# Kernel optimization log

Measured on AMD Instinct MI355X. Metric: run time of the kernel, lower is better.

The kernel has to match this reference:

```python
import jax, jax.numpy as jnp
import numpy as np

N = 100_000          # nodes
E = 1_600_000        # edges
NUM_LABELS = 1000
LBL_DIM = 64
BBOX_DIM = 64        # bbox MLP output dim
HID = 128            # gnn hidden = out channels; gnn in = LBL_DIM + BBOX_DIM = 128


def setup_inputs() -> dict:
    key = jax.random.key(0)
    ks = jax.random.split(key, 14)
    label = jax.random.randint(ks[0], (N,), 0, NUM_LABELS)
    bbox = jax.random.uniform(ks[1], (N, 4), dtype=jnp.float32)
    edge_index = jax.random.randint(ks[2], (2, E), 0, N)
    emb_table = jax.random.normal(ks[3], (NUM_LABELS, LBL_DIM), dtype=jnp.float32) * 0.02
    mlp_w1 = jax.random.normal(ks[4], (4, BBOX_DIM), dtype=jnp.float32) * 0.5
    mlp_b1 = jnp.zeros((BBOX_DIM,), jnp.float32)
    mlp_w2 = jax.random.normal(ks[5], (BBOX_DIM, BBOX_DIM), dtype=jnp.float32) * 0.125
    mlp_b2 = jnp.zeros((BBOX_DIM,), jnp.float32)
    w_g0 = jax.random.normal(ks[6], (HID, HID), dtype=jnp.float32) * 0.088
    b_g0 = jnp.zeros((HID,), jnp.float32)
    w_g1 = jax.random.normal(ks[7], (HID, HID), dtype=jnp.float32) * 0.088
    b_g1 = jnp.zeros((HID,), jnp.float32)
    w_g2 = jax.random.normal(ks[8], (HID, HID), dtype=jnp.float32) * 0.088
    b_g2 = jnp.zeros((HID,), jnp.float32)
    return dict(label=label, bbox=bbox, edge_index=edge_index, emb_table=emb_table,
                mlp_w1=mlp_w1, mlp_b1=mlp_b1, mlp_w2=mlp_w2, mlp_b2=mlp_b2,
                w_g0=w_g0, b_g0=b_g0, w_g1=w_g1, b_g1=b_g1, w_g2=w_g2, b_g2=b_g2)


def _gcn_norm(edge_index, n):
    # add self loops, compute symmetric normalization deg^-1/2 A_hat deg^-1/2
    loops = jnp.arange(n, dtype=edge_index.dtype)
    src = jnp.concatenate([edge_index[0], loops])
    dst = jnp.concatenate([edge_index[1], loops])
    deg = jax.ops.segment_sum(jnp.ones_like(dst, dtype=jnp.float32), dst, num_segments=n)
    dinv = jnp.where(deg > 0, jax.lax.rsqrt(deg), 0.0)
    norm = dinv[src] * dinv[dst]  # [E+N]
    return src, dst, norm


def _gcn_conv(x, src, dst, norm, w, b, n):
    h = x @ w                                   # [N, C]
    msg = h[src] * norm[:, None]                # gather + scale, [E+N, C]
    out = jax.ops.segment_sum(msg, dst, num_segments=n)  # scatter-add
    return out + b


def reference(label, bbox, edge_index, emb_table,
              mlp_w1, mlp_b1, mlp_w2, mlp_b2,
              w_g0, b_g0, w_g1, b_g1, w_g2, b_g2):
    n = bbox.shape[0]
    lbl = emb_table[label]                                  # [N, 64]
    h = jax.nn.relu(bbox @ mlp_w1 + mlp_b1) @ mlp_w2 + mlp_b2  # [N, 64]
    x = jnp.concatenate([lbl, h], axis=-1)                  # [N, 128]
    src, dst, norm = _gcn_norm(edge_index, n)
    x = jax.nn.relu(_gcn_conv(x, src, dst, norm, w_g0, b_g0, n))
    x = jax.nn.relu(_gcn_conv(x, src, dst, norm, w_g1, b_g1, n))
    x = _gcn_conv(x, src, dst, norm, w_g2, b_g2, n)
    return x
```

## Files before the change

### kernel.cpp

```cpp
#include <hip/hip_runtime.h>
#include <hip/hip_bf16.h>
#include <hip/hip_fp16.h>
#include <cstdint>
#include <cstddef>

typedef _Float16 h8 __attribute__((ext_vector_type(8)));
typedef float f4 __attribute__((ext_vector_type(4)));

#define CNT_PAD 16


__global__ __launch_bounds__(256) void k_count_rank(const int* __restrict__ dst, int* __restrict__ cnt_pad,
                                                    int* __restrict__ rank, int E) {
    int i = blockIdx.x * 256 + threadIdx.x;
    if (i < E) rank[i] = atomicAdd(&cnt_pad[(size_t)dst[i] * CNT_PAD], 1);
}

__global__ __launch_bounds__(256) void k_scan_a(const int* __restrict__ cnt_pad, int* __restrict__ offs,
                                                int* __restrict__ partials, float* __restrict__ dinv,
                                                int* __restrict__ blockHist, int N, int nb) {
    __shared__ int sh[256];
    __shared__ int lh[64];
    int t = threadIdx.x;
    if (t < 64) lh[t] = 0;
    int i = blockIdx.x * 256 + t;
    int v = (i < N) ? (cnt_pad[(size_t)i * CNT_PAD] + 1) : 0;
    sh[t] = v;
    __syncthreads();
    if (i < N) {
        int b = v < 64 ? v : 63;
        atomicAdd(&lh[b], 1);
    }
    for (int d = 1; d < 256; d <<= 1) {
        int add = (t >= d) ? sh[t - d] : 0;
        __syncthreads();
        sh[t] += add;
        __syncthreads();
    }
    if (i < N) {
        offs[i] = sh[t] - v;
        dinv[i] = rsqrtf((float)v);
    }
    if (t == 255) partials[blockIdx.x] = sh[255];
    __syncthreads();
    if (t < 64) blockHist[(size_t)t * nb + blockIdx.x] = lh[t];
}

__global__ __launch_bounds__(256) void k_scan_bins(int* __restrict__ blockHist, int* __restrict__ hist, int nb) {
    __shared__ int sh[256];
    int b = blockIdx.x;
    int* p = blockHist + (size_t)b * nb;
    int t = threadIdx.x;
    int carry = 0;
    for (int base = 0; base < nb; base += 256) {
        int idx = base + t;
        int v = idx < nb ? p[idx] : 0;
        sh[t] = v;
        __syncthreads();
        for (int d = 1; d < 256; d <<= 1) {
            int add = (t >= d) ? sh[t - d] : 0;
            __syncthreads();
            sh[t] += add;
            __syncthreads();
        }
        if (idx < nb) p[idx] = carry + sh[t] - v;
        carry += sh[255];
        __syncthreads();
    }
    if (t == 0) hist[b * CNT_PAD] = carry;
}

__global__ __launch_bounds__(512) void k_scan_b(int* __restrict__ partials, int* __restrict__ hist, int nb) {
    __shared__ int sh[512];
    __shared__ int hs[64];
    int t = threadIdx.x;
    int v = (t < nb) ? partials[t] : 0;
    sh[t] = v;
    if (t < 64) hs[t] = hist[t * CNT_PAD];
    __syncthreads();
    for (int d = 1; d < 512; d <<= 1) {
        int add = (t >= d) ? sh[t - d] : 0;
        __syncthreads();
        sh[t] += add;
        __syncthreads();
    }
    if (t < nb) partials[t] = sh[t];
    for (int d = 1; d < 64; d <<= 1) {
        int add = (t >= d && t < 64) ? hs[t - d] : 0;
        __syncthreads();
        if (t < 64) hs[t] += add;
        __syncthreads();
    }
    if (t < 64) hist[t * CNT_PAD] = t ? hs[t - 1] : 0;
}

__global__ __launch_bounds__(256) void k_scan_c(int* __restrict__ offs, const int* __restrict__ partials,
                                                const int* __restrict__ cnt_pad, const float* __restrict__ dinv,
                                                long long* __restrict__ cpack, int N, int nb) {
    int i = blockIdx.x * 256 + threadIdx.x;
    if (i < N) {
        int b = i >> 8;
        int o = offs[i] + (b > 0 ? partials[b - 1] : 0);
        offs[i] = o;
        int cnt = cnt_pad[(size_t)i * CNT_PAD];
        float di = dinv[i];
        unsigned int nrm = (unsigned int)__float_as_int(di * di);
        long long v = ((long long)nrm << 32) | (unsigned int)i;
        __builtin_nontemporal_store(v, &cpack[o + cnt]);
    } else if (i == N) {
        offs[N] = partials[nb - 1];
    }
}

__global__ __launch_bounds__(256) void k_fill2(const int* __restrict__ src, const int* __restrict__ dst,
                                               const int* __restrict__ rank, const int* __restrict__ offs,
                                               const float* __restrict__ dinv,
                                               long long* __restrict__ cpack, int E) {
    int i = blockIdx.x * 256 + threadIdx.x;
    if (i < E) {
        int s = src[i], d = dst[i];
        int pos = offs[d] + rank[i];
        unsigned int nrm = (unsigned int)__float_as_int(dinv[s] * dinv[d]);
        long long v = ((long long)nrm << 32) | (unsigned int)s;
        __builtin_nontemporal_store(v, &cpack[pos]);
    }
}

__global__ __launch_bounds__(256) void k_perm_scatter2(const int* __restrict__ cnt_pad,
                                                       const int* __restrict__ hist,
                                                       const int* __restrict__ blockBinOff,
                                                       int* __restrict__ perm, int N, int nb) {
    __shared__ int lh[64];
    int t = threadIdx.x;
    if (t < 64) lh[t] = 0;
    __syncthreads();
    int i = blockIdx.x * 256 + t;
    if (i < N) {
        int deg = cnt_pad[(size_t)i * CNT_PAD] + 1;
        int b = deg < 64 ? deg : 63;
        int lr = atomicAdd(&lh[b], 1);
        int pos = hist[b * CNT_PAD] + blockBinOff[(size_t)b * nb + blockIdx.x] + lr;
        perm[pos] = i;
    }
}


__global__ __launch_bounds__(256) void k_prep_w(const float* __restrict__ w0, const float* __restrict__ w1,
                                                const float* __restrict__ w2, _Float16* __restrict__ WT) {
    int idx = blockIdx.x * 256 + threadIdx.x;
    if (idx >= 3 * 16384) return;
    int l = idx >> 14, rem = idx & 16383, c = rem >> 7, k = rem & 127;
    const float* W = (l == 0) ? w0 : (l == 1) ? w1 : w2;
    WT[idx] = (_Float16)W[k * 128 + c];
}


__global__ __launch_bounds__(256) void k_feat_gemm(const int* __restrict__ label, const float* __restrict__ bbox,
                                                   const float* __restrict__ emb,
                                                   const float* __restrict__ w1, const float* __restrict__ b1,
                                                   const float* __restrict__ w2, const float* __restrict__ b2,
                                                   const _Float16* __restrict__ WT0,
                                                   _Float16* __restrict__ G0, int N) {
    __shared__ float w1s[256];
    __shared__ float b1s[64], b2s[64];
    __shared__ _Float16 w2t[64][72];
    __shared__ _Float16 h1s[32][72];
    __shared__ _Float16 Fl[32][136];

    int t = threadIdx.x;
    if (t < 256) w1s[t] = w1[t];
    if (t < 64) { b1s[t] = b1[t]; b2s[t] = b2[t]; }
    #pragma unroll
    for (int i = 0; i < 16; ++i) {
        int idx = t + i * 256;
        int k = idx >> 6, c = idx & 63;
        w2t[c][k] = (_Float16)w2[idx];
    }

    int wv = t >> 6, lane = t & 63;
    int r = lane & 15, q = lane >> 4;
    int blockBase = blockIdx.x * 32;
    int nb0 = blockBase + wv * 8;

    #pragma unroll
    for (int nn = 0; nn < 8; ++nn) {
        int node = nb0 + nn;
        float h1 = 0.f;
        _Float16 ev = (_Float16)0.f;
        if (node < N) {
            float bb0 = bbox[node * 4 + 0];
            float bb1 = bbox[node * 4 + 1];
            float bb2 = bbox[node * 4 + 2];
            float bb3 = bbox[node * 4 + 3];
            h1 = fmaxf(bb0 * w1s[lane] + bb1 * w1s[64 + lane]
                     + bb2 * w1s[128 + lane] + bb3 * w1s[192 + lane] + b1s[lane], 0.f);
            ev = (_Float16)emb[(size_t)label[node] * 64 + lane];
        }
        h1s[wv * 8 + nn][lane] = (_Float16)h1;
        Fl[wv * 8 + nn][lane] = ev;
    }
    __syncthreads();

    int rt = wv & 1, ch = wv >> 1;
    {
        h8 a0 = *(const h8*)&h1s[rt * 16 + r][q * 8];
        h8 a1 = *(const h8*)&h1s[rt * 16 + r][32 + q * 8];
        #pragma unroll
        for (int ct = 0; ct < 2; ++ct) {
            int col = ch * 32 + ct * 16 + r;
            h8 bv0 = *(const h8*)&w2t[col][q * 8];
            h8 bv1 = *(const h8*)&w2t[col][32 + q * 8];
            f4 acc = {0.f, 0.f, 0.f, 0.f};
            acc = __builtin_amdgcn_mfma_f32_16x16x32_f16(a0, bv0, acc, 0, 0, 0);
            acc = __builtin_amdgcn_mfma_f32_16x16x32_f16(a1, bv1, acc, 0, 0, 0);
            float bb = b2s[col];
            #pragma unroll
            for (int i = 0; i < 4; ++i)
                Fl[rt * 16 + q * 4 + i][64 + col] = (_Float16)(acc[i] + bb);
        }
    }
    __syncthreads();

    {
        h8 a[4];
        #pragma unroll
        for (int s = 0; s < 4; ++s) a[s] = *(const h8*)&Fl[rt * 16 + r][s * 32 + q * 8];
        #pragma unroll
        for (int ct = 0; ct < 4; ++ct) {
            int col = ch * 64 + ct * 16 + r;
            f4 acc = {0.f, 0.f, 0.f, 0.f};
            #pragma unroll
            for (int s = 0; s < 4; ++s) {
                h8 bv = *(const h8*)&WT0[(size_t)col * 128 + s * 32 + q * 8];
                acc = __builtin_amdgcn_mfma_f32_16x16x32_f16(a[s], bv, acc, 0, 0, 0);
            }
            #pragma unroll
            for (int i = 0; i < 4; ++i) {
                int node = blockBase + rt * 16 + q * 4 + i;
                if (node < N) G0[(size_t)node * 128 + col] = (_Float16)acc[i];
            }
        }
    }
}


__global__ __launch_bounds__(256) void k_gemm_mfma(const _Float16* __restrict__ X,
                                                   const _Float16* __restrict__ WT,
                                                   _Float16* __restrict__ H, int N) {
    int t = threadIdx.x;
    int wv = t >> 6, lane = t & 63;
    int r = lane & 15, q = lane >> 4;
    int n0 = blockIdx.x * 64 + wv * 16;

    int arow = n0 + r; if (arow > N - 1) arow = N - 1;
    h8 a[4];
    #pragma unroll
    for (int s = 0; s < 4; ++s)
        a[s] = *(const h8*)&X[(size_t)arow * 128 + s * 32 + q * 8];

    #pragma unroll
    for (int ct = 0; ct < 8; ++ct) {
        h8 b[4];
        #pragma unroll
        for (int s = 0; s < 4; ++s)
            b[s] = *(const h8*)&WT[(size_t)(ct * 16 + r) * 128 + s * 32 + q * 8];
        f4 acc = {0.f, 0.f, 0.f, 0.f};
        #pragma unroll
        for (int s = 0; s < 4; ++s)
            acc = __builtin_amdgcn_mfma_f32_16x16x32_f16(a[s], b[s], acc, 0, 0, 0);
        #pragma unroll
        for (int i = 0; i < 4; ++i) {
            int row = n0 + q * 4 + i;
            if (row < N) H[(size_t)row * 128 + ct * 16 + r] = (_Float16)acc[i];
        }
    }
}


#define FMA8(hv, wv_)                                                                        \
    {                                                                                        \
        float2 f;                                                                            \
        f = __half22float2(*(const __half2*)&(hv).x); acc[0] += f.x * (wv_); acc[1] += f.y * (wv_); \
        f = __half22float2(*(const __half2*)&(hv).y); acc[2] += f.x * (wv_); acc[3] += f.y * (wv_); \
        f = __half22float2(*(const __half2*)&(hv).z); acc[4] += f.x * (wv_); acc[5] += f.y * (wv_); \
        f = __half22float2(*(const __half2*)&(hv).w); acc[6] += f.x * (wv_); acc[7] += f.y * (wv_); \
    }

template <int OUT_HALF>
__global__ __launch_bounds__(256) void k_agg(const uint4* __restrict__ H4, const int* __restrict__ offs,
                                             const int2* __restrict__ cpack, const int* __restrict__ perm,
                                             const float* __restrict__ bias, void* __restrict__ Yv,
                                             int N, int do_relu) {
    int slot = blockIdx.x * 16 + (threadIdx.x >> 4);
    if (slot >= N) return;
    int node = perm[slot];
    int li = threadIdx.x & 15;
    int i0 = offs[node], i1 = offs[node + 1];

    float acc[8];
    #pragma unroll
    for (int k = 0; k < 8; ++k) acc[k] = 0.f;

    for (int base = i0; base < i1; base += 16) {
        int navail = i1 - base; if (navail > 16) navail = 16;
        int lidx = li < navail ? li : (navail - 1);
        int2 ep = cpack[base + lidx];

        float wA[4]; uint4 hA[4];
        #pragma unroll
        for (int j = 0; j < 4; ++j) {
            int cl = j < navail ? j : (navail - 1);
            int s = __shfl(ep.x, cl, 16);
            float wj = __int_as_float(__shfl(ep.y, cl, 16));
            wA[j] = j < navail ? wj : 0.f;
            hA[j] = H4[(size_t)s * 16 + li];
        }
        for (int e = 4; e < navail; e += 4) {
            float wB[4]; uint4 hB[4];
            #pragma unroll
            for (int j = 0; j < 4; ++j) {
                int idx = e + j;
                int cl = idx < navail ? idx : (navail - 1);
                int s = __shfl(ep.x, cl, 16);
                float wj = __int_as_float(__shfl(ep.y, cl, 16));
                wB[j] = idx < navail ? wj : 0.f;
                hB[j] = H4[(size_t)s * 16 + li];
            }
            #pragma unroll
            for (int j = 0; j < 4; ++j) FMA8(hA[j], wA[j]);
            #pragma unroll
            for (int j = 0; j < 4; ++j) { wA[j] = wB[j]; hA[j] = hB[j]; }
        }
        #pragma unroll
        for (int j = 0; j < 4; ++j) FMA8(hA[j], wA[j]);
    }

    float4 b0 = *(const float4*)&bias[li * 8];
    float4 b1 = *(const float4*)&bias[li * 8 + 4];
    acc[0] += b0.x; acc[1] += b0.y; acc[2] += b0.z; acc[3] += b0.w;
    acc[4] += b1.x; acc[5] += b1.y; acc[6] += b1.z; acc[7] += b1.w;
    if (do_relu) {
        #pragma unroll
        for (int k = 0; k < 8; ++k) acc[k] = fmaxf(acc[k], 0.f);
    }
    if (OUT_HALF) {
        __half2 p0 = __float22half2_rn(make_float2(acc[0], acc[1]));
        __half2 p1 = __float22half2_rn(make_float2(acc[2], acc[3]));
        __half2 p2 = __float22half2_rn(make_float2(acc[4], acc[5]));
        __half2 p3 = __float22half2_rn(make_float2(acc[6], acc[7]));
        uint4 pk;
        pk.x = *(unsigned int*)&p0; pk.y = *(unsigned int*)&p1;
        pk.z = *(unsigned int*)&p2; pk.w = *(unsigned int*)&p3;
        ((uint4*)Yv)[(size_t)node * 16 + li] = pk;
    } else {
        float* Yf = (float*)Yv;
        *(float4*)&Yf[(size_t)node * 128 + li * 8]     = make_float4(acc[0], acc[1], acc[2], acc[3]);
        *(float4*)&Yf[(size_t)node * 128 + li * 8 + 4] = make_float4(acc[4], acc[5], acc[6], acc[7]);
    }
}


extern "C" void kernel_launch(void* const* d_in, const int* in_sizes, int n_in,
                              void* d_out, int out_size, void* d_ws, size_t ws_size,
                              hipStream_t stream) {
    const int*   label = (const int*)d_in[0];
    const float* bbox  = (const float*)d_in[1];
    const int*   eidx  = (const int*)d_in[2];
    const float* emb   = (const float*)d_in[3];
    const float* w1    = (const float*)d_in[4];
    const float* b1    = (const float*)d_in[5];
    const float* w2    = (const float*)d_in[6];
    const float* b2    = (const float*)d_in[7];
    const float* wg0   = (const float*)d_in[8];
    const float* bg0   = (const float*)d_in[9];
    const float* wg1   = (const float*)d_in[10];
    const float* bg1   = (const float*)d_in[11];
    const float* wg2   = (const float*)d_in[12];
    const float* bg2   = (const float*)d_in[13];

    int N = in_sizes[0];
    int E = in_sizes[2] / 2;
    const int* esrc = eidx;
    const int* edst = eidx + E;

    char* ws = (char*)d_ws;
    int*       offs      = (int*)      (ws + 0x000000);
    float*     dinv      = (float*)    (ws + 0x070000);
    int*       perm      = (int*)      (ws + 0x0E0000);
    int*       partials  = (int*)      (ws + 0x150000);
    int*       hist      = (int*)      (ws + 0x158000);
    _Float16*  WT        = (_Float16*) (ws + 0x160000);
    int*       blockBinOff = (int*)    (ws + 0x180000);
    long long* cpack     = (long long*)(ws + 0x200000);
    __half*    B         = (__half*)   (ws + 0x1000000);
    int*       cnt_pad   = (int*)      (ws + 0x1000000);
    int*       rank      = (int*)      (ws + 0x1800000);
    __half*    A         = (__half*)   (ws + 0x2900000);
    float*     Of        = (float*)    d_out;

    int nb = (N + 255) / 256;
    int eb = (E + 255) / 256;

    hipMemsetAsync(cnt_pad, 0, (size_t)N * CNT_PAD * 4, stream);
    k_count_rank<<<eb, 256, 0, stream>>>(edst, cnt_pad, rank, E);
    k_scan_a<<<nb, 256, 0, stream>>>(cnt_pad, offs, partials, dinv, blockBinOff, N, nb);
    k_scan_bins<<<64, 256, 0, stream>>>(blockBinOff, hist, nb);
    k_scan_b<<<1, 512, 0, stream>>>(partials, hist, nb);
    k_scan_c<<<(N + 1 + 255) / 256, 256, 0, stream>>>(offs, partials, cnt_pad, dinv, cpack, N, nb);
    k_fill2<<<eb, 256, 0, stream>>>(esrc, edst, rank, offs, dinv, cpack, E);
    k_perm_scatter2<<<nb, 256, 0, stream>>>(cnt_pad, hist, blockBinOff, perm, N, nb);

    k_prep_w<<<192, 256, 0, stream>>>(wg0, wg1, wg2, WT);
    k_feat_gemm<<<(N + 31) / 32, 256, 0, stream>>>(label, bbox, emb, w1, b1, w2, b2,
                                                   WT + 0 * 16384, (_Float16*)A, N);

    int gemm_grid = (N + 63) / 64;
    int agg_grid  = (N + 15) / 16;

    k_agg<1><<<agg_grid, 256, 0, stream>>>((const uint4*)A, offs, (const int2*)cpack, perm, bg0, B, N, 1);
    k_gemm_mfma<<<gemm_grid, 256, 0, stream>>>((const _Float16*)B, WT + 1 * 16384, (_Float16*)A, N);
    k_agg<1><<<agg_grid, 256, 0, stream>>>((const uint4*)A, offs, (const int2*)cpack, perm, bg1, B, N, 1);
    k_gemm_mfma<<<gemm_grid, 256, 0, stream>>>((const _Float16*)B, WT + 2 * 16384, (_Float16*)A, N);
    k_agg<0><<<agg_grid, 256, 0, stream>>>((const uint4*)A, offs, (const int2*)cpack, perm, bg2, Of, N, 0);
}
```

Baseline: 441.8 us.

## Fuse GCN aggregation with next-layer MFMA GEMM and batch edge preprocessing

```diff
diff --git a/kernel.cpp b/kernel.cpp
--- a/kernel.cpp
+++ b/kernel.cpp
@@ -12,8 +12,22 @@
 
 __global__ __launch_bounds__(256) void k_count_rank(const int* __restrict__ dst, int* __restrict__ cnt_pad,
                                                     int* __restrict__ rank, int E) {
-    int i = blockIdx.x * 256 + threadIdx.x;
-    if (i < E) rank[i] = atomicAdd(&cnt_pad[(size_t)dst[i] * CNT_PAD], 1);
+    int G = gridDim.x * 256;
+    int g = blockIdx.x * 256 + threadIdx.x;
+    int idx[4], d[4]; bool v[4];
+    #pragma unroll
+    for (int k = 0; k < 4; ++k) {
+        idx[k] = g + k * G;
+        v[k] = idx[k] < E;
+        d[k] = v[k] ? dst[idx[k]] : 0;
+    }
+    int r[4];
+    #pragma unroll
+    for (int k = 0; k < 4; ++k)
+        if (v[k]) r[k] = atomicAdd(&cnt_pad[(size_t)d[k] * CNT_PAD], 1);
+    #pragma unroll
+    for (int k = 0; k < 4; ++k)
+        if (v[k]) rank[idx[k]] = r[k];
 }
 
 __global__ __launch_bounds__(256) void k_scan_a(const int* __restrict__ cnt_pad, int* __restrict__ offs,
@@ -116,13 +130,29 @@
                                                const int* __restrict__ rank, const int* __restrict__ offs,
                                                const float* __restrict__ dinv,
                                                long long* __restrict__ cpack, int E) {
-    int i = blockIdx.x * 256 + threadIdx.x;
-    if (i < E) {
-        int s = src[i], d = dst[i];
-        int pos = offs[d] + rank[i];
-        unsigned int nrm = (unsigned int)__float_as_int(dinv[s] * dinv[d]);
-        long long v = ((long long)nrm << 32) | (unsigned int)s;
-        __builtin_nontemporal_store(v, &cpack[pos]);
+    int G = gridDim.x * 256;
+    int g = blockIdx.x * 256 + threadIdx.x;
+    int idx[4], s[4], d[4], rk[4]; bool v[4];
+    #pragma unroll
+    for (int k = 0; k < 4; ++k) {
+        idx[k] = g + k * G;
+        v[k] = idx[k] < E;
+        int safe = v[k] ? idx[k] : 0;
+        s[k] = src[safe]; d[k] = dst[safe]; rk[k] = rank[safe];
+    }
+    int pos[4]; float ds[4], dd[4];
+    #pragma unroll
+    for (int k = 0; k < 4; ++k) {
+        pos[k] = offs[d[k]] + rk[k];
+        ds[k] = dinv[s[k]]; dd[k] = dinv[d[k]];
+    }
+    #pragma unroll
+    for (int k = 0; k < 4; ++k) {
+        if (v[k]) {
+            unsigned int nrm = (unsigned int)__float_as_int(ds[k] * dd[k]);
+            long long val = ((long long)nrm << 32) | (unsigned int)s[k];
+            __builtin_nontemporal_store(val, &cpack[pos[k]]);
+        }
     }
 }
 
@@ -244,39 +274,6 @@
 }
 
 
-__global__ __launch_bounds__(256) void k_gemm_mfma(const _Float16* __restrict__ X,
-                                                   const _Float16* __restrict__ WT,
-                                                   _Float16* __restrict__ H, int N) {
-    int t = threadIdx.x;
-    int wv = t >> 6, lane = t & 63;
-    int r = lane & 15, q = lane >> 4;
-    int n0 = blockIdx.x * 64 + wv * 16;
-
-    int arow = n0 + r; if (arow > N - 1) arow = N - 1;
-    h8 a[4];
-    #pragma unroll
-    for (int s = 0; s < 4; ++s)
-        a[s] = *(const h8*)&X[(size_t)arow * 128 + s * 32 + q * 8];
-
-    #pragma unroll
-    for (int ct = 0; ct < 8; ++ct) {
-        h8 b[4];
-        #pragma unroll
-        for (int s = 0; s < 4; ++s)
-            b[s] = *(const h8*)&WT[(size_t)(ct * 16 + r) * 128 + s * 32 + q * 8];
-        f4 acc = {0.f, 0.f, 0.f, 0.f};
-        #pragma unroll
-        for (int s = 0; s < 4; ++s)
-            acc = __builtin_amdgcn_mfma_f32_16x16x32_f16(a[s], b[s], acc, 0, 0, 0);
-        #pragma unroll
-        for (int i = 0; i < 4; ++i) {
-            int row = n0 + q * 4 + i;
-            if (row < N) H[(size_t)row * 128 + ct * 16 + r] = (_Float16)acc[i];
-        }
-    }
-}
-
-
 #define FMA8(hv, wv_)                                                                        \
     {                                                                                        \
         float2 f;                                                                            \
@@ -286,76 +283,109 @@
         f = __half22float2(*(const __half2*)&(hv).w); acc[6] += f.x * (wv_); acc[7] += f.y * (wv_); \
     }
 
-template <int OUT_HALF>
-__global__ __launch_bounds__(256) void k_agg(const uint4* __restrict__ H4, const int* __restrict__ offs,
-                                             const int2* __restrict__ cpack, const int* __restrict__ perm,
-                                             const float* __restrict__ bias, void* __restrict__ Yv,
-                                             int N, int do_relu) {
-    int slot = blockIdx.x * 16 + (threadIdx.x >> 4);
-    if (slot >= N) return;
-    int node = perm[slot];
-    int li = threadIdx.x & 15;
-    int i0 = offs[node], i1 = offs[node + 1];
+template <int MODE>
+__global__ __launch_bounds__(256) void k_agg_gemm(const uint4* __restrict__ H4, const int* __restrict__ offs,
+                                                  const int2* __restrict__ cpack,
+                                                  const int* __restrict__ perm,
+                                                  const float* __restrict__ bias,
+                                                  const _Float16* __restrict__ WTnext,
+                                                  void* __restrict__ Yv, int N) {
+    __shared__ _Float16 Zl[16][136];
+    __shared__ int nid[16];
+
+    int t = threadIdx.x;
+    int grp = t >> 4;
+    int li = t & 15;
+    int blockBase = blockIdx.x * 16;
+    int slot = blockBase + grp;
+    int node;
+    if (MODE == 1) node = slot < N ? perm[slot] : -1;
+    else           node = slot < N ? slot : -1;
+    if (MODE == 1 && li == 0) nid[grp] = node;
 
     float acc[8];
     #pragma unroll
     for (int k = 0; k < 8; ++k) acc[k] = 0.f;
 
-    for (int base = i0; base < i1; base += 16) {
-        int navail = i1 - base; if (navail > 16) navail = 16;
-        int lidx = li < navail ? li : (navail - 1);
-        int2 ep = cpack[base + lidx];
-
-        float wA[4]; uint4 hA[4];
-        #pragma unroll
-        for (int j = 0; j < 4; ++j) {
-            int cl = j < navail ? j : (navail - 1);
-            int s = __shfl(ep.x, cl, 16);
-            float wj = __int_as_float(__shfl(ep.y, cl, 16));
-            wA[j] = j < navail ? wj : 0.f;
-            hA[j] = H4[(size_t)s * 16 + li];
-        }
-        for (int e = 4; e < navail; e += 4) {
-            float wB[4]; uint4 hB[4];
+    if (node >= 0) {
+        int i0 = offs[node], i1 = offs[node + 1];
+        for (int base = i0; base < i1; base += 16) {
+            int navail = i1 - base; if (navail > 16) navail = 16;
+            int lidx = li < navail ? li : (navail - 1);
+            int2 ep = cpack[base + lidx];
+
+            float wA[4]; uint4 hA[4];
             #pragma unroll
             for (int j = 0; j < 4; ++j) {
-                int idx = e + j;
-                int cl = idx < navail ? idx : (navail - 1);
+                int cl = j < navail ? j : (navail - 1);
                 int s = __shfl(ep.x, cl, 16);
                 float wj = __int_as_float(__shfl(ep.y, cl, 16));
-                wB[j] = idx < navail ? wj : 0.f;
-                hB[j] = H4[(size_t)s * 16 + li];
+                wA[j] = j < navail ? wj : 0.f;
+                hA[j] = H4[(size_t)s * 16 + li];
+            }
+            for (int e = 4; e < navail; e += 4) {
+                float wB[4]; uint4 hB[4];
+                #pragma unroll
+                for (int j = 0; j < 4; ++j) {
+                    int idx = e + j;
+                    int cl = idx < navail ? idx : (navail - 1);
+                    int s = __shfl(ep.x, cl, 16);
+                    float wj = __int_as_float(__shfl(ep.y, cl, 16));
+                    wB[j] = idx < navail ? wj : 0.f;
+                    hB[j] = H4[(size_t)s * 16 + li];
+                }
+                #pragma unroll
+                for (int j = 0; j < 4; ++j) FMA8(hA[j], wA[j]);
+                #pragma unroll
+                for (int j = 0; j < 4; ++j) { wA[j] = wB[j]; hA[j] = hB[j]; }
             }
             #pragma unroll
             for (int j = 0; j < 4; ++j) FMA8(hA[j], wA[j]);
-            #pragma unroll
-            for (int j = 0; j < 4; ++j) { wA[j] = wB[j]; hA[j] = hB[j]; }
-        }
-        #pragma unroll
-        for (int j = 0; j < 4; ++j) FMA8(hA[j], wA[j]);
+        }
     }
 
     float4 b0 = *(const float4*)&bias[li * 8];
     float4 b1 = *(const float4*)&bias[li * 8 + 4];
     acc[0] += b0.x; acc[1] += b0.y; acc[2] += b0.z; acc[3] += b0.w;
     acc[4] += b1.x; acc[5] += b1.y; acc[6] += b1.z; acc[7] += b1.w;
-    if (do_relu) {
-        #pragma unroll
-        for (int k = 0; k < 8; ++k) acc[k] = fmaxf(acc[k], 0.f);
-    }
-    if (OUT_HALF) {
-        __half2 p0 = __float22half2_rn(make_float2(acc[0], acc[1]));
-        __half2 p1 = __float22half2_rn(make_float2(acc[2], acc[3]));
-        __half2 p2 = __float22half2_rn(make_float2(acc[4], acc[5]));
-        __half2 p3 = __float22half2_rn(make_float2(acc[6], acc[7]));
-        uint4 pk;
-        pk.x = *(unsigned int*)&p0; pk.y = *(unsigned int*)&p1;
-        pk.z = *(unsigned int*)&p2; pk.w = *(unsigned int*)&p3;
-        ((uint4*)Yv)[(size_t)node * 16 + li] = pk;
-    } else {
-        float* Yf = (float*)Yv;
-        *(float4*)&Yf[(size_t)node * 128 + li * 8]     = make_float4(acc[0], acc[1], acc[2], acc[3]);
-        *(float4*)&Yf[(size_t)node * 128 + li * 8 + 4] = make_float4(acc[4], acc[5], acc[6], acc[7]);
+
+    if (MODE == 0) {
+        if (node >= 0) {
+            float* Yf = (float*)Yv;
+            *(float4*)&Yf[(size_t)node * 128 + li * 8]     = make_float4(acc[0], acc[1], acc[2], acc[3]);
+            *(float4*)&Yf[(size_t)node * 128 + li * 8 + 4] = make_float4(acc[4], acc[5], acc[6], acc[7]);
+        }
+        return;
+    }
+
+    {
+        h8 fr;
+        #pragma unroll
+        for (int k = 0; k < 8; ++k) fr[k] = (_Float16)fmaxf(acc[k], 0.f);
+        *(h8*)&Zl[grp][li * 8] = fr;
+    }
+    __syncthreads();
+
+    int wv = t >> 6, lane = t & 63;
+    int r = lane & 15, q = lane >> 4;
+    _Float16* G = (_Float16*)Yv;
+    h8 a[4];
+    #pragma unroll
+    for (int s = 0; s < 4; ++s) a[s] = *(const h8*)&Zl[r][s * 32 + q * 8];
+    #pragma unroll
+    for (int ct2 = 0; ct2 < 2; ++ct2) {
+        int col = (wv * 2 + ct2) * 16 + r;
+        f4 gacc = {0.f, 0.f, 0.f, 0.f};
+        #pragma unroll
+        for (int s = 0; s < 4; ++s) {
+            h8 bv = *(const h8*)&WTnext[(size_t)col * 128 + s * 32 + q * 8];
+            gacc = __builtin_amdgcn_mfma_f32_16x16x32_f16(a[s], bv, gacc, 0, 0, 0);
+        }
+        #pragma unroll
+        for (int i = 0; i < 4; ++i) {
+            int nrow = nid[q * 4 + i];
+            if (nrow >= 0) G[(size_t)nrow * 128 + col] = (_Float16)gacc[i];
+        }
     }
 }
 
@@ -386,12 +416,12 @@
     char* ws = (char*)d_ws;
     int*       offs      = (int*)      (ws + 0x000000);
     float*     dinv      = (float*)    (ws + 0x070000);
-    int*       perm      = (int*)      (ws + 0x0E0000);
     int*       partials  = (int*)      (ws + 0x150000);
     int*       hist      = (int*)      (ws + 0x158000);
     _Float16*  WT        = (_Float16*) (ws + 0x160000);
     int*       blockBinOff = (int*)    (ws + 0x180000);
-    long long* cpack     = (long long*)(ws + 0x200000);
+    int*       perm      = (int*)      (ws + 0x1A0000);
+    long long* cpack     = (long long*)(ws + 0x280000);
     __half*    B         = (__half*)   (ws + 0x1000000);
     int*       cnt_pad   = (int*)      (ws + 0x1000000);
     int*       rank      = (int*)      (ws + 0x1800000);
@@ -399,27 +429,27 @@
     float*     Of        = (float*)    d_out;
 
     int nb = (N + 255) / 256;
-    int eb = (E + 255) / 256;
+    int eb4 = (E + 1023) / 1024;
 
     hipMemsetAsync(cnt_pad, 0, (size_t)N * CNT_PAD * 4, stream);
-    k_count_rank<<<eb, 256, 0, stream>>>(edst, cnt_pad, rank, E);
+    k_count_rank<<<eb4, 256, 0, stream>>>(edst, cnt_pad, rank, E);
     k_scan_a<<<nb, 256, 0, stream>>>(cnt_pad, offs, partials, dinv, blockBinOff, N, nb);
     k_scan_bins<<<64, 256, 0, stream>>>(blockBinOff, hist, nb);
     k_scan_b<<<1, 512, 0, stream>>>(partials, hist, nb);
     k_scan_c<<<(N + 1 + 255) / 256, 256, 0, stream>>>(offs, partials, cnt_pad, dinv, cpack, N, nb);
-    k_fill2<<<eb, 256, 0, stream>>>(esrc, edst, rank, offs, dinv, cpack, E);
+    k_fill2<<<eb4, 256, 0, stream>>>(esrc, edst, rank, offs, dinv, cpack, E);
     k_perm_scatter2<<<nb, 256, 0, stream>>>(cnt_pad, hist, blockBinOff, perm, N, nb);
 
     k_prep_w<<<192, 256, 0, stream>>>(wg0, wg1, wg2, WT);
     k_feat_gemm<<<(N + 31) / 32, 256, 0, stream>>>(label, bbox, emb, w1, b1, w2, b2,
                                                    WT + 0 * 16384, (_Float16*)A, N);
 
-    int gemm_grid = (N + 63) / 64;
-    int agg_grid  = (N + 15) / 16;
-
-    k_agg<1><<<agg_grid, 256, 0, stream>>>((const uint4*)A, offs, (const int2*)cpack, perm, bg0, B, N, 1);
-    k_gemm_mfma<<<gemm_grid, 256, 0, stream>>>((const _Float16*)B, WT + 1 * 16384, (_Float16*)A, N);
-    k_agg<1><<<agg_grid, 256, 0, stream>>>((const uint4*)A, offs, (const int2*)cpack, perm, bg1, B, N, 1);
-    k_gemm_mfma<<<gemm_grid, 256, 0, stream>>>((const _Float16*)B, WT + 2 * 16384, (_Float16*)A, N);
-    k_agg<0><<<agg_grid, 256, 0, stream>>>((const uint4*)A, offs, (const int2*)cpack, perm, bg2, Of, N, 0);
-}
+    int agg_grid = (N + 15) / 16;
+
+    k_agg_gemm<1><<<agg_grid, 256, 0, stream>>>((const uint4*)A, offs, (const int2*)cpack, perm, bg0,
+                                                WT + 1 * 16384, B, N);
+    k_agg_gemm<1><<<agg_grid, 256, 0, stream>>>((const uint4*)B, offs, (const int2*)cpack, perm, bg1,
+                                                WT + 2 * 16384, A, N);
+    k_agg_gemm<0><<<agg_grid, 256, 0, stream>>>((const uint4*)A, offs, (const int2*)cpack, nullptr, bg2,
+                                                nullptr, Of, N);
+}
```

Result: faster. 386.2 us (-12.6%).
